# Optimization experiments

Measured on AMD Instinct MI355X. Metric: run time of the kernel, lower is better.

The kernel has to match this reference:

```python
import jax, jax.numpy as jnp
import numpy as np

H = 32        # query heads
KV = 8        # kv heads (GQA)
D = 128       # head_dim
HID = 4096    # hidden_size
T = 2048      # tokens (single causal sequence)
THETA = 10000.0


def setup_inputs() -> dict:
    key = jax.random.key(0)
    k1, k2, k3 = jax.random.split(key, 3)
    return {
        "positions": jnp.arange(T, dtype=jnp.int32),
        "hidden_states": jax.random.normal(k1, (T, HID), dtype=jnp.float32),
        "w_qkv": jax.random.normal(k2, ((H + 2 * KV) * D, HID), dtype=jnp.float32) * 0.02,
        "w_o": jax.random.normal(k3, (HID, H * D), dtype=jnp.float32) * 0.02,
    }


def _rope_neox(x, cos, sin):
    # x: [T, h, D]; cos/sin: [T, D/2]
    half = x.shape[-1] // 2
    x1, x2 = x[..., :half], x[..., half:]
    c, s = cos[:, None, :], sin[:, None, :]
    return jnp.concatenate([x1 * c - x2 * s, x2 * c + x1 * s], axis=-1)


def reference(positions, hidden_states, w_qkv, w_o):
    t = hidden_states.shape[0]
    qkv = hidden_states @ w_qkv.T                      # [T, (H+2KV)*D]
    q, k, v = jnp.split(qkv, [H * D, H * D + KV * D], axis=-1)
    q = q.reshape(t, H, D)
    k = k.reshape(t, KV, D)
    v = v.reshape(t, KV, D)

    # neox-style RoPE over full head_dim
    half = D // 2
    inv_freq = 1.0 / (THETA ** (jnp.arange(0, D, 2, dtype=jnp.float32) / D))  # [D/2]
    freqs = positions.astype(jnp.float32)[:, None] * inv_freq                 # [T, D/2]
    cos, sin = jnp.cos(freqs), jnp.sin(freqs)
    q = _rope_neox(q, cos, sin)
    k = _rope_neox(k, cos, sin)

    # GQA: expand kv heads to match query heads
    rep = H // KV
    k = jnp.repeat(k, rep, axis=1)                     # [T, H, D]
    v = jnp.repeat(v, rep, axis=1)

    scale = D ** -0.5
    scores = jnp.einsum('thd,shd->hts', q, k) * scale  # [H, T, T]
    causal = positions[:, None] >= positions[None, :]  # [T, T]
    neg = jnp.finfo(scores.dtype).min
    scores = jnp.where(causal[None], scores, neg)
    attn = jax.nn.softmax(scores, axis=-1)
    out = jnp.einsum('hts,shd->thd', attn, v).reshape(t, H * D)
    return out @ w_o.T                                 # [T, HID]
```

## Files before the change

kernel.cpp:

```cpp
#include <hip/hip_runtime.h>
#include <hip/hip_bf16.h>
#include <cstdint>

typedef __bf16 bf16;
typedef __bf16 bf16x8 __attribute__((ext_vector_type(8)));
typedef float f32x4 __attribute__((ext_vector_type(4)));

#define DEV __device__ __forceinline__

DEV f32x4 mfma16(bf16x8 a, bf16x8 b, f32x4 c) {
  return __builtin_amdgcn_mfma_f32_16x16x32_bf16(a, b, c, 0, 0, 0);
}

DEV void gl2lds16(const void* g, void* l) {
  __builtin_amdgcn_global_load_lds((__attribute__((address_space(1))) void*)g,
                                   (__attribute__((address_space(3))) void*)l,
                                   16, 0, 0);
}

#define VMWAIT(N) asm volatile("s_waitcnt vmcnt(" #N ")" ::: "memory")

DEV void cvt8(const float* __restrict__ s, bf16* __restrict__ d) {
  f32x4 a = *(const f32x4*)(s);
  f32x4 b = *(const f32x4*)(s + 4);
  bf16x8 o;
#pragma unroll
  for (int e = 0; e < 4; ++e) { o[e] = (bf16)a[e]; o[e + 4] = (bf16)b[e]; }
  *(bf16x8*)(d) = o;
}

__global__ void cvt3(const float* __restrict__ s0, bf16* __restrict__ d0, int n0,
                     const float* __restrict__ s1, bf16* __restrict__ d1, int n1,
                     const float* __restrict__ s2, bf16* __restrict__ d2) {
  long i = ((long)blockIdx.x * 256 + threadIdx.x) * 8;
  if (i < n0) { cvt8(s0 + i, d0 + i); return; }
  i -= n0;
  if (i < n1) { cvt8(s1 + i, d1 + i); return; }
  i -= n1;
  cvt8(s2 + i, d2 + i);
}

template <typename OutT, int SPLIT>
DEV void gemm256_body(const bf16* __restrict__ A, const bf16* __restrict__ B,
                      OutT* __restrict__ C, int M, int N, int K) {
  __shared__ char lds[131072];
  const int tid = threadIdx.x;
  const int lane = tid & 63, w = tid >> 6;
  const int wm = w >> 2, wn = w & 3;
  const int quad = lane >> 4, r = lane & 15;
  const long mBase = (long)blockIdx.y * 256, nBase = (long)blockIdx.x * 256;
  const int Kh = K / SPLIT;
  const long kBeg = (long)blockIdx.z * Kh;
  const int G = Kh >> 5;

  const bf16* src[4];
#pragma unroll
  for (int i = 0; i < 4; ++i) {
    const int c = i * 512 + tid;
    const int part = c >> 10, row = (c >> 2) & 255, slot = c & 3;
    const int kc = slot ^ ((row >> 1) & 3);
    const bf16* base = part ? (B + (nBase + row) * (long)K)
                            : (A + (mBase + row) * (long)K);
    src[i] = base + kBeg + kc * 8;
  }

  const int pslot = (quad ^ ((r >> 1) & 3)) << 4;
  const int offA = (wm * 128 + r) * 64 + pslot;
  const int offB = 16384 + (wn * 64 + r) * 64 + pslot;

  f32x4 acc[8][4];
#pragma unroll
  for (int i = 0; i < 8; ++i)
#pragma unroll
    for (int j = 0; j < 4; ++j) acc[i][j] = f32x4{0.f, 0.f, 0.f, 0.f};

  auto stage = [&](int p) {
    char* db = lds + ((p & 3) << 15);
    const long ko = (long)p * 32;
#pragma unroll
    for (int i = 0; i < 4; ++i)
      gl2lds16(src[i] + ko, db + (i * 512 + w * 64) * 16);
  };

  auto phase = [&](int p, bool do_stage) {
    __builtin_amdgcn_s_barrier();
    __builtin_amdgcn_sched_barrier(0);
    char* rb = lds + ((p & 3) << 15);
    bf16x8 af[8], bfr[4];
#pragma unroll
    for (int mi = 0; mi < 8; ++mi) af[mi] = *(const bf16x8*)(rb + offA + mi * 1024);
#pragma unroll
    for (int ni = 0; ni < 4; ++ni) bfr[ni] = *(const bf16x8*)(rb + offB + ni * 1024);
    if (do_stage) stage(p + 3);
    asm volatile("s_waitcnt lgkmcnt(0)" ::: "memory");
    __builtin_amdgcn_sched_barrier(0);
    __builtin_amdgcn_s_setprio(1);
#pragma unroll
    for (int mi = 0; mi < 8; ++mi)
#pragma unroll
      for (int ni = 0; ni < 4; ++ni)
        acc[mi][ni] = mfma16(af[mi], bfr[ni], acc[mi][ni]);
    __builtin_amdgcn_s_setprio(0);
  };

  stage(0); stage(1); stage(2);
  for (int p = 0; p < G - 3; ++p) { VMWAIT(8); phase(p, true); }
  VMWAIT(8); phase(G - 3, false);
  VMWAIT(4); phase(G - 2, false);
  VMWAIT(0); phase(G - 1, false);

  OutT* Cz = C + (size_t)blockIdx.z * M * N;
#pragma unroll
  for (int mi = 0; mi < 8; ++mi)
#pragma unroll
    for (int ni = 0; ni < 4; ++ni)
#pragma unroll
      for (int rg = 0; rg < 4; ++rg) {
        long row = mBase + wm * 128 + mi * 16 + quad * 4 + rg;
        long col = nBase + wn * 64 + ni * 16 + r;
        Cz[row * N + col] = (OutT)acc[mi][ni][rg];
      }
}

__global__ __launch_bounds__(512, 2) void gemm_qkv(const bf16* __restrict__ A,
                                                   const bf16* __restrict__ B,
                                                   bf16* __restrict__ C, int M, int N, int K) {
  gemm256_body<bf16, 1>(A, B, C, M, N, K);
}

__global__ __launch_bounds__(512, 2) void gemm_out2(const bf16* __restrict__ A,
                                                    const bf16* __restrict__ B,
                                                    float* __restrict__ C, int M, int N, int K) {
  gemm256_body<float, 2>(A, B, C, M, N, K);
}

__global__ void reduce_add(const float* __restrict__ p, float* __restrict__ o, int n) {
  const int i = (blockIdx.x * 256 + threadIdx.x) * 8;
  const f32x4 a0 = *(const f32x4*)(p + i),     b0 = *(const f32x4*)(p + n + i);
  const f32x4 a1 = *(const f32x4*)(p + i + 4), b1 = *(const f32x4*)(p + n + i + 4);
  *(f32x4*)(o + i) = a0 + b0;
  *(f32x4*)(o + i + 4) = a1 + b1;
}

__global__ void rope_kernel(bf16* __restrict__ qkv, const int* __restrict__ pos) {
  int idx = blockIdx.x * 256 + threadIdx.x;
  int g = idx & 7;
  int rest = idx >> 3;
  int head = rest % 40;
  int t = rest / 40;
  bf16* p = qkv + (long)t * 6144 + head * 128 + g * 8;
  bf16x8 a = *(const bf16x8*)(p);
  bf16x8 b = *(const bf16x8*)(p + 64);
  const float pf = (float)pos[t];
  bf16x8 oa, ob;
#pragma unroll
  for (int e = 0; e < 8; ++e) {
    const int d = g * 8 + e;
    const float invf = __builtin_expf(-(float)d * (9.210340371976184f / 64.0f));
    const float fr = pf * invf;
    const float c = __builtin_cosf(fr), s = __builtin_sinf(fr);
    const float x1 = (float)a[e], x2 = (float)b[e];
    oa[e] = (bf16)(x1 * c - x2 * s);
    ob[e] = (bf16)(x2 * c + x1 * s);
  }
  *(bf16x8*)(p) = oa;
  *(bf16x8*)(p + 64) = ob;
}

__global__ __launch_bounds__(256, 2) void attn_kernel(const bf16* __restrict__ qkv,
                                                      bf16* __restrict__ out) {
  constexpr int LDV = 72, LDP = 72;
  constexpr float SCL2 = 0.08838834764831845f * 1.4426950408889634f;
  __shared__ bf16 Ks[2][64 * 128];
  __shared__ bf16 Vt[2][128 * LDV];
  __shared__ bf16 Ps[64 * LDP];
  const int tid = threadIdx.x;
  const int lane = tid & 63, w = tid >> 6;
  const int quad = lane >> 4, r = lane & 15;
  const int pr = blockIdx.x, h = blockIdx.y;
  const int kvh = h >> 2;

  bf16x8 kreg[4], vreg[4];
  int srow[4], sdc[4];
#pragma unroll
  for (int ii = 0; ii < 4; ++ii) {
    const int c = ii * 256 + tid;
    srow[ii] = c >> 4;
    sdc[ii] = c & 15;
  }

  for (int which = 0; which < 2; ++which) {
    const int qt = which ? (31 - pr) : pr;
    const int rowq = qt * 64 + w * 16;

    bf16x8 qf[4];
#pragma unroll
    for (int ks = 0; ks < 4; ++ks)
      qf[ks] = *(const bf16x8*)(qkv + (long)(rowq + r) * 6144 + h * 128 + ks * 32 + quad * 8);

    f32x4 of[8];
#pragma unroll
    for (int di = 0; di < 8; ++di) of[di] = f32x4{0.f, 0.f, 0.f, 0.f};
    float mrun[4], lrun[4];
#pragma unroll
    for (int rg = 0; rg < 4; ++rg) { mrun[rg] = -__builtin_inff(); lrun[rg] = 0.f; }

    const int ntiles = qt + 1;
#pragma unroll
    for (int ii = 0; ii < 4; ++ii) {
      const long rb = (long)srow[ii] * 6144 + kvh * 128;
      kreg[ii] = *(const bf16x8*)(qkv + rb + 4096 + sdc[ii] * 8);
      vreg[ii] = *(const bf16x8*)(qkv + rb + 5120 + sdc[ii] * 8);
    }

    for (int kt = 0; kt < ntiles; ++kt) {
      const int kvbase = kt * 64;
      const int buf = kt & 1;
#pragma unroll
      for (int ii = 0; ii < 4; ++ii) {
        const int row = srow[ii], dc = sdc[ii];
        *(bf16x8*)(&Ks[buf][row * 128 + ((dc ^ (row & 15)) << 3)]) = kreg[ii];
        const int pc = (((row >> 3) ^ (dc & 7)) << 3) + (row & 7);
#pragma unroll
        for (int e = 0; e < 8; ++e) Vt[buf][(dc * 8 + e) * LDV + pc] = vreg[ii][e];
      }
      {
        const int kvn = (kt + 1 < ntiles) ? (kt + 1) * 64 : kt * 64;
#pragma unroll
        for (int ii = 0; ii < 4; ++ii) {
          const long rb = (long)(kvn + srow[ii]) * 6144 + kvh * 128;
          kreg[ii] = *(const bf16x8*)(qkv + rb + 4096 + sdc[ii] * 8);
          vreg[ii] = *(const bf16x8*)(qkv + rb + 5120 + sdc[ii] * 8);
        }
      }
      __syncthreads();

      f32x4 sacc[4];
#pragma unroll
      for (int ni = 0; ni < 4; ++ni) sacc[ni] = f32x4{0.f, 0.f, 0.f, 0.f};
#pragma unroll
      for (int ks = 0; ks < 4; ++ks) {
        bf16x8 kf[4];
#pragma unroll
        for (int ni = 0; ni < 4; ++ni)
          kf[ni] = *(const bf16x8*)(&Ks[buf][(ni * 16 + r) * 128 + (((ks * 4 + quad) ^ r) << 3)]);
#pragma unroll
        for (int ni = 0; ni < 4; ++ni) sacc[ni] = mfma16(qf[ks], kf[ni], sacc[ni]);
      }

      float mt[4];
#pragma unroll
      for (int rg = 0; rg < 4; ++rg) mt[rg] = -1e30f;
      if (kt == qt) {
        const int rq = rowq + quad * 4;
#pragma unroll
        for (int ni = 0; ni < 4; ++ni) {
          const int ck = kvbase + ni * 16 + r;
#pragma unroll
          for (int rg = 0; rg < 4; ++rg) {
            float sv = sacc[ni][rg];
            sv = (ck > rq + rg) ? -1e30f : sv;
            sacc[ni][rg] = sv;
            mt[rg] = fmaxf(mt[rg], sv);
          }
        }
      } else {
#pragma unroll
        for (int ni = 0; ni < 4; ++ni)
#pragma unroll
          for (int rg = 0; rg < 4; ++rg) mt[rg] = fmaxf(mt[rg], sacc[ni][rg]);
      }
#pragma unroll
      for (int rg = 0; rg < 4; ++rg) {
        float v = mt[rg];
        v = fmaxf(v, __shfl_xor(v, 1));
        v = fmaxf(v, __shfl_xor(v, 2));
        v = fmaxf(v, __shfl_xor(v, 4));
        v = fmaxf(v, __shfl_xor(v, 8));
        mt[rg] = v;
      }
      float alpha[4], rsum[4];
#pragma unroll
      for (int rg = 0; rg < 4; ++rg) {
        const float mnew = fmaxf(mrun[rg], mt[rg]);
        alpha[rg] = __builtin_exp2f((mrun[rg] - mnew) * SCL2);
        mrun[rg] = mnew;
        rsum[rg] = 0.f;
      }
#pragma unroll
      for (int ni = 0; ni < 4; ++ni)
#pragma unroll
        for (int rg = 0; rg < 4; ++rg) {
          const float pv = __builtin_exp2f((sacc[ni][rg] - mrun[rg]) * SCL2);
          rsum[rg] += pv;
          Ps[(w * 16 + quad * 4 + rg) * LDP + ni * 16 + r] = (bf16)pv;
        }
#pragma unroll
      for (int rg = 0; rg < 4; ++rg) {
        float v = rsum[rg];
        v += __shfl_xor(v, 1);
        v += __shfl_xor(v, 2);
        v += __shfl_xor(v, 4);
        v += __shfl_xor(v, 8);
        lrun[rg] = lrun[rg] * alpha[rg] + v;
      }
#pragma unroll
      for (int di = 0; di < 8; ++di)
#pragma unroll
        for (int rg = 0; rg < 4; ++rg) of[di][rg] *= alpha[rg];

#pragma unroll
      for (int js = 0; js < 2; ++js) {
        const bf16x8 pf = *(const bf16x8*)(&Ps[(w * 16 + r) * LDP + js * 32 + quad * 8]);
#pragma unroll
        for (int di = 0; di < 8; ++di) {
          const int vrow = di * 16 + r;
          const int vcol = (((js * 4 + quad) ^ ((vrow >> 3) & 7)) << 3);
          const bf16x8 vf = *(const bf16x8*)(&Vt[buf][vrow * LDV + vcol]);
          of[di] = mfma16(pf, vf, of[di]);
        }
      }
    }

#pragma unroll
    for (int rg = 0; rg < 4; ++rg) {
      const float inv = 1.f / lrun[rg];
      const long t = rowq + quad * 4 + rg;
#pragma unroll
      for (int di = 0; di < 8; ++di)
        out[t * 4096 + h * 128 + di * 16 + r] = (bf16)(of[di][rg] * inv);
    }
  }
}

extern "C" void kernel_launch(void* const* d_in, const int* in_sizes, int n_in,
                              void* d_out, int out_size, void* d_ws, size_t ws_size,
                              hipStream_t stream) {
  const int* positions = (const int*)d_in[0];
  const float* hidden = (const float*)d_in[1];
  const float* w_qkv = (const float*)d_in[2];
  const float* w_o = (const float*)d_in[3];
  float* out = (float*)d_out;

  char* ws = (char*)d_ws;
  bf16* hid_b  = (bf16*)(ws);
  bf16* wqkv_b = (bf16*)(ws + 16777216);
  bf16* wo_b   = (bf16*)(ws + 67108864);
  bf16* qkv    = (bf16*)(ws + 100663296);
  bf16* attn   = (bf16*)(ws + 125829120);
  float* part  = (float*)(ws);

  cvt3<<<24576, 256, 0, stream>>>(hidden, hid_b, 8388608,
                                  w_qkv, wqkv_b, 25165824,
                                  w_o, wo_b);
  gemm_qkv<<<dim3(24, 8), 512, 0, stream>>>(hid_b, wqkv_b, qkv, 2048, 6144, 4096);
  rope_kernel<<<2560, 256, 0, stream>>>(qkv, positions);
  attn_kernel<<<dim3(16, 32), 256, 0, stream>>>(qkv, attn);
  gemm_out2<<<dim3(16, 8, 2), 512, 0, stream>>>(attn, wo_b, part, 2048, 4096, 4096);
  reduce_add<<<4096, 256, 0, stream>>>(part, out, 8388608);
}
```

Before: 549.1 us.

## Replace split-K output GEMM plus reduce with 128x256-tile GEMM; add attention setprio

The output projection previously used 256x256 tiles with split-K=2, writing fp32 partials and then running a separate reduction kernel. It now uses a dedicated 128x256-tile kernel with full K, giving 256 blocks that write the final fp32 output directly. This removes the partial-sum traffic and the extra launch, but each block reads its B tile over a smaller M tile, so operand reuse per block is lower. The attention kernel also raises wave priority around its MFMA loops.

Result: faster. 525.5 us (-4.3%).

```diff
diff --git a/kernel.cpp b/kernel.cpp
--- a/kernel.cpp
+++ b/kernel.cpp
@@ -40,18 +40,16 @@
   cvt8(s2 + i, d2 + i);
 }
 
-template <typename OutT, int SPLIT>
-DEV void gemm256_body(const bf16* __restrict__ A, const bf16* __restrict__ B,
-                      OutT* __restrict__ C, int M, int N, int K) {
+__global__ __launch_bounds__(512, 2) void gemm_qkv(const bf16* __restrict__ A,
+                                                   const bf16* __restrict__ B,
+                                                   bf16* __restrict__ C, int M, int N, int K) {
   __shared__ char lds[131072];
   const int tid = threadIdx.x;
   const int lane = tid & 63, w = tid >> 6;
   const int wm = w >> 2, wn = w & 3;
   const int quad = lane >> 4, r = lane & 15;
   const long mBase = (long)blockIdx.y * 256, nBase = (long)blockIdx.x * 256;
-  const int Kh = K / SPLIT;
-  const long kBeg = (long)blockIdx.z * Kh;
-  const int G = Kh >> 5;
+  const int G = K >> 5;
 
   const bf16* src[4];
 #pragma unroll
@@ -61,7 +59,7 @@
     const int kc = slot ^ ((row >> 1) & 3);
     const bf16* base = part ? (B + (nBase + row) * (long)K)
                             : (A + (mBase + row) * (long)K);
-    src[i] = base + kBeg + kc * 8;
+    src[i] = base + kc * 8;
   }
 
   const int pslot = (quad ^ ((r >> 1) & 3)) << 4;
@@ -109,7 +107,6 @@
   VMWAIT(4); phase(G - 2, false);
   VMWAIT(0); phase(G - 1, false);
 
-  OutT* Cz = C + (size_t)blockIdx.z * M * N;
 #pragma unroll
   for (int mi = 0; mi < 8; ++mi)
 #pragma unroll
@@ -118,28 +115,89 @@
       for (int rg = 0; rg < 4; ++rg) {
         long row = mBase + wm * 128 + mi * 16 + quad * 4 + rg;
         long col = nBase + wn * 64 + ni * 16 + r;
-        Cz[row * N + col] = (OutT)acc[mi][ni][rg];
-      }
-}
-
-__global__ __launch_bounds__(512, 2) void gemm_qkv(const bf16* __restrict__ A,
+        C[row * N + col] = (bf16)acc[mi][ni][rg];
+      }
+}
+
+__global__ __launch_bounds__(512, 2) void gemm_out(const bf16* __restrict__ A,
                                                    const bf16* __restrict__ B,
-                                                   bf16* __restrict__ C, int M, int N, int K) {
-  gemm256_body<bf16, 1>(A, B, C, M, N, K);
-}
-
-__global__ __launch_bounds__(512, 2) void gemm_out2(const bf16* __restrict__ A,
-                                                    const bf16* __restrict__ B,
-                                                    float* __restrict__ C, int M, int N, int K) {
-  gemm256_body<float, 2>(A, B, C, M, N, K);
-}
-
-__global__ void reduce_add(const float* __restrict__ p, float* __restrict__ o, int n) {
-  const int i = (blockIdx.x * 256 + threadIdx.x) * 8;
-  const f32x4 a0 = *(const f32x4*)(p + i),     b0 = *(const f32x4*)(p + n + i);
-  const f32x4 a1 = *(const f32x4*)(p + i + 4), b1 = *(const f32x4*)(p + n + i + 4);
-  *(f32x4*)(o + i) = a0 + b0;
-  *(f32x4*)(o + i + 4) = a1 + b1;
+                                                   float* __restrict__ C, int M, int N, int K) {
+  __shared__ char lds[98304];
+  const int tid = threadIdx.x;
+  const int lane = tid & 63, w = tid >> 6;
+  const int wm = w >> 2, wn = w & 3;
+  const int quad = lane >> 4, r = lane & 15;
+  const long mBase = (long)blockIdx.y * 128, nBase = (long)blockIdx.x * 256;
+  const int G = K >> 5;
+
+  const bf16* src[3];
+#pragma unroll
+  for (int i = 0; i < 3; ++i) {
+    const int c = i * 512 + tid;
+    const int partB = (c >= 512);
+    const int rb = partB ? (c - 512) : c;
+    const int row = rb >> 2, slot = rb & 3;
+    const int kc = slot ^ ((row >> 1) & 3);
+    const bf16* base = partB ? (B + (nBase + row) * (long)K)
+                             : (A + (mBase + row) * (long)K);
+    src[i] = base + kc * 8;
+  }
+
+  const int pslot = (quad ^ ((r >> 1) & 3)) << 4;
+  const int offA = (wm * 64 + r) * 64 + pslot;
+  const int offB = 8192 + (wn * 64 + r) * 64 + pslot;
+
+  f32x4 acc[4][4];
+#pragma unroll
+  for (int i = 0; i < 4; ++i)
+#pragma unroll
+    for (int j = 0; j < 4; ++j) acc[i][j] = f32x4{0.f, 0.f, 0.f, 0.f};
+
+  auto stage = [&](int p) {
+    char* db = lds + (p & 3) * 24576;
+    const long ko = (long)p * 32;
+    gl2lds16(src[0] + ko, db + (w * 64) * 16);
+    gl2lds16(src[1] + ko, db + 8192 + (w * 64) * 16);
+    gl2lds16(src[2] + ko, db + 8192 + (512 + w * 64) * 16);
+  };
+
+  auto phase = [&](int p, bool do_stage) {
+    __builtin_amdgcn_s_barrier();
+    __builtin_amdgcn_sched_barrier(0);
+    char* rbuf = lds + (p & 3) * 24576;
+    bf16x8 af[4], bfr[4];
+#pragma unroll
+    for (int mi = 0; mi < 4; ++mi) af[mi] = *(const bf16x8*)(rbuf + offA + mi * 1024);
+#pragma unroll
+    for (int ni = 0; ni < 4; ++ni) bfr[ni] = *(const bf16x8*)(rbuf + offB + ni * 1024);
+    if (do_stage) stage(p + 3);
+    asm volatile("s_waitcnt lgkmcnt(0)" ::: "memory");
+    __builtin_amdgcn_sched_barrier(0);
+    __builtin_amdgcn_s_setprio(1);
+#pragma unroll
+    for (int mi = 0; mi < 4; ++mi)
+#pragma unroll
+      for (int ni = 0; ni < 4; ++ni)
+        acc[mi][ni] = mfma16(af[mi], bfr[ni], acc[mi][ni]);
+    __builtin_amdgcn_s_setprio(0);
+  };
+
+  stage(0); stage(1); stage(2);
+  for (int p = 0; p < G - 3; ++p) { VMWAIT(6); phase(p, true); }
+  VMWAIT(6); phase(G - 3, false);
+  VMWAIT(3); phase(G - 2, false);
+  VMWAIT(0); phase(G - 1, false);
+
+#pragma unroll
+  for (int mi = 0; mi < 4; ++mi)
+#pragma unroll
+    for (int ni = 0; ni < 4; ++ni)
+#pragma unroll
+      for (int rg = 0; rg < 4; ++rg) {
+        long row = mBase + wm * 64 + mi * 16 + quad * 4 + rg;
+        long col = nBase + wn * 64 + ni * 16 + r;
+        C[row * N + col] = acc[mi][ni][rg];
+      }
 }
 
 __global__ void rope_kernel(bf16* __restrict__ qkv, const int* __restrict__ pos) {
@@ -238,6 +296,7 @@
       f32x4 sacc[4];
 #pragma unroll
       for (int ni = 0; ni < 4; ++ni) sacc[ni] = f32x4{0.f, 0.f, 0.f, 0.f};
+      __builtin_amdgcn_s_setprio(1);
 #pragma unroll
       for (int ks = 0; ks < 4; ++ks) {
         bf16x8 kf[4];
@@ -247,6 +306,7 @@
 #pragma unroll
         for (int ni = 0; ni < 4; ++ni) sacc[ni] = mfma16(qf[ks], kf[ni], sacc[ni]);
       }
+      __builtin_amdgcn_s_setprio(0);
 
       float mt[4];
 #pragma unroll
@@ -309,6 +369,7 @@
 #pragma unroll
         for (int rg = 0; rg < 4; ++rg) of[di][rg] *= alpha[rg];
 
+      __builtin_amdgcn_s_setprio(1);
 #pragma unroll
       for (int js = 0; js < 2; ++js) {
         const bf16x8 pf = *(const bf16x8*)(&Ps[(w * 16 + r) * LDP + js * 32 + quad * 8]);
@@ -320,6 +381,7 @@
           of[di] = mfma16(pf, vf, of[di]);
         }
       }
+      __builtin_amdgcn_s_setprio(0);
     }
 
 #pragma unroll
@@ -348,7 +410,6 @@
   bf16* wo_b   = (bf16*)(ws + 67108864);
   bf16* qkv    = (bf16*)(ws + 100663296);
   bf16* attn   = (bf16*)(ws + 125829120);
-  float* part  = (float*)(ws);
 
   cvt3<<<24576, 256, 0, stream>>>(hidden, hid_b, 8388608,
                                   w_qkv, wqkv_b, 25165824,
@@ -356,6 +417,5 @@
   gemm_qkv<<<dim3(24, 8), 512, 0, stream>>>(hid_b, wqkv_b, qkv, 2048, 6144, 4096);
   rope_kernel<<<2560, 256, 0, stream>>>(qkv, positions);
   attn_kernel<<<dim3(16, 32), 256, 0, stream>>>(qkv, attn);
-  gemm_out2<<<dim3(16, 8, 2), 512, 0, stream>>>(attn, wo_b, part, 2048, 4096, 4096);
-  reduce_add<<<4096, 256, 0, stream>>>(part, out, 8388608);
-}
+  gemm_out<<<dim3(16, 16), 512, 0, stream>>>(attn, wo_b, out, 2048, 4096, 4096);
+}
```
